# Performance work log

Hardware: AMD Instinct MI355X
Metric: run time of the kernel (lower is better)

The kernel has to match this reference:

```python
import jax, jax.numpy as jnp
import numpy as np


def _lstm_dir(x, Wih, Whh, bih, bhh, reverse):
    # x: [B,T,D]; Wih: [4H,D]; Whh: [4H,H]; PyTorch gate order i,f,g,o
    if reverse:
        x = x[:, ::-1, :]
    H = Whh.shape[1]
    B = x.shape[0]
    # precompute input projection for all timesteps: [B,T,4H]
    xW = jnp.einsum('btd,gd->btg', x, Wih) + bih + bhh
    xW = jnp.swapaxes(xW, 0, 1)  # [T,B,4H]
    h0 = jnp.zeros((B, H), x.dtype)
    c0 = jnp.zeros((B, H), x.dtype)

    def step(carry, xt):
        h, c = carry
        g = xt + h @ Whh.T
        i, f, gg, o = jnp.split(g, 4, axis=-1)
        c = jax.nn.sigmoid(f) * c + jax.nn.sigmoid(i) * jnp.tanh(gg)
        h = jax.nn.sigmoid(o) * jnp.tanh(c)
        return (h, c), h

    _, ys = jax.lax.scan(step, (h0, c0), xW)
    ys = jnp.swapaxes(ys, 0, 1)  # [B,T,H]
    if reverse:
        ys = ys[:, ::-1, :]
    return ys


def _bilstm(x, Wih_f, Whh_f, bih_f, bhh_f, Wih_b, Whh_b, bih_b, bhh_b):
    yf = _lstm_dir(x, Wih_f, Whh_f, bih_f, bhh_f, False)
    yb = _lstm_dir(x, Wih_b, Whh_b, bih_b, bhh_b, True)
    return jnp.concatenate([yf, yb], axis=-1)


def setup_inputs() -> dict:
    key = jax.random.key(0)
    B, T, D = 1024, 512, 30
    H1, H2, DENSE, OUT = 96, 64, 32, 1
    ks = jax.random.split(key, 21)

    def U(k, shape, fan):
        bnd = 1.0 / np.sqrt(fan)
        return jax.random.uniform(k, shape, jnp.float32, -bnd, bnd)

    x = jax.random.normal(ks[0], (B, T, D), jnp.float32)
    inp = {'x': x}
    # layer 1 (input D -> H1), forward and backward directions
    inp['Wih1f'] = U(ks[1], (4 * H1, D), H1)
    inp['Whh1f'] = U(ks[2], (4 * H1, H1), H1)
    inp['bih1f'] = U(ks[3], (4 * H1,), H1)
    inp['bhh1f'] = U(ks[4], (4 * H1,), H1)
    inp['Wih1b'] = U(ks[5], (4 * H1, D), H1)
    inp['Whh1b'] = U(ks[6], (4 * H1, H1), H1)
    inp['bih1b'] = U(ks[7], (4 * H1,), H1)
    inp['bhh1b'] = U(ks[8], (4 * H1,), H1)
    # layer 2 (input 2*H1 -> H2)
    inp['Wih2f'] = U(ks[9], (4 * H2, 2 * H1), H2)
    inp['Whh2f'] = U(ks[10], (4 * H2, H2), H2)
    inp['bih2f'] = U(ks[11], (4 * H2,), H2)
    inp['bhh2f'] = U(ks[12], (4 * H2,), H2)
    inp['Wih2b'] = U(ks[13], (4 * H2, 2 * H1), H2)
    inp['Whh2b'] = U(ks[14], (4 * H2, H2), H2)
    inp['bih2b'] = U(ks[15], (4 * H2,), H2)
    inp['bhh2b'] = U(ks[16], (4 * H2,), H2)
    # dense head
    inp['W1'] = U(ks[17], (DENSE, 2 * H2), 2 * H2)
    inp['b1'] = U(ks[18], (DENSE,), 2 * H2)
    inp['W2'] = U(ks[19], (OUT, DENSE), DENSE)
    inp['b2'] = U(ks[20], (OUT,), DENSE)
    return inp


def reference(x, Wih1f, Whh1f, bih1f, bhh1f, Wih1b, Whh1b, bih1b, bhh1b,
              Wih2f, Whh2f, bih2f, bhh2f, Wih2b, Whh2b, bih2b, bhh2b,
              W1, b1, W2, b2):
    # dropout layers are identity in eval mode
    h1 = _bilstm(x, Wih1f, Whh1f, bih1f, bhh1f, Wih1b, Whh1b, bih1b, bhh1b)   # [B,T,192]
    h2 = _bilstm(h1, Wih2f, Whh2f, bih2f, bhh2f, Wih2b, Whh2b, bih2b, bhh2b)  # [B,T,128]
    last = h2[:, -1, :]                       # [B,128]
    d = jax.nn.relu(last @ W1.T + b1)         # [B,32]
    return d @ W2.T + b2                      # [B,1]
```

## Files before the change

### kernel.cpp

```cpp
#include <hip/hip_runtime.h>
#include <math.h>

#define B_  1024
#define T_  512
#define D_  30
#define H1_ 96
#define G1_ 384
#define H2_ 64
#define G2_ 256

__device__ float g_h1[(size_t)B_ * T_ * 192];
__device__ float g_h2f[(size_t)B_ * H2_];

__device__ __forceinline__ float fast_tanh(float v) {
  float a = fabsf(v);
  float e = __expf(-2.0f * a);
  float t = 1.0f - 2.0f * e / (1.0f + e);
  return v < 0.0f ? -t : t;
}
__device__ __forceinline__ float fast_sigmoid(float v) {
  return 0.5f + 0.5f * fast_tanh(0.5f * v);
}

#define FMAROW(a_, w_, v_)                                                    \
  a_ = fmaf(w_.x, v_.x, a_); a_ = fmaf(w_.y, v_.y, a_);                       \
  a_ = fmaf(w_.z, v_.z, a_); a_ = fmaf(w_.w, v_.w, a_);

#define BAR_LGKM() do {                                                       \
    asm volatile("s_waitcnt lgkmcnt(0)" ::: "memory");                        \
    __builtin_amdgcn_s_barrier();                                             \
    asm volatile("" ::: "memory");                                            \
  } while (0)

__global__ __launch_bounds__(768, 4)
void lstm1_kernel(const float* __restrict__ x,
                  const float* __restrict__ Wih_f, const float* __restrict__ Whh_f,
                  const float* __restrict__ bih_f, const float* __restrict__ bhh_f,
                  const float* __restrict__ Wih_b, const float* __restrict__ Whh_b,
                  const float* __restrict__ bih_b, const float* __restrict__ bhh_b)
{
  const int tid = threadIdx.x;
  const int dir = blockIdx.y;
  const int b0  = blockIdx.x * 8;

  const float* __restrict__ Wih = dir ? Wih_b : Wih_f;
  const float* __restrict__ Whh = dir ? Whh_b : Whh_f;
  const float* __restrict__ bih = dir ? bih_b : bih_f;
  const float* __restrict__ bhh = dir ? bhh_b : bhh_f;

  const int j  = tid >> 3;
  const int e  = tid & 7;
  const int wv = tid >> 6;
  const int jl = j & 7;

  __shared__ __align__(16) float hxs[2 * 1056];
  __shared__ float4 scr4[12 * 584];

  float4 wA0,wA1,wA2,wA3, wB0,wB1,wB2,wB3, wC0,wC1,wC2,wC3, wD0,wD1,wD2,wD3;
  if (e < 2) {
    const int k0 = e * 16;
#define LDXF(r_, kk) (((kk) < D_) ? Wih[(r_) * D_ + (kk)] : 0.0f)
#define LW4(d0,d1,d2,d3, r_) {                                                \
    d0 = make_float4(LDXF(r_,k0+ 0),LDXF(r_,k0+ 1),LDXF(r_,k0+ 2),LDXF(r_,k0+ 3)); \
    d1 = make_float4(LDXF(r_,k0+ 4),LDXF(r_,k0+ 5),LDXF(r_,k0+ 6),LDXF(r_,k0+ 7)); \
    d2 = make_float4(LDXF(r_,k0+ 8),LDXF(r_,k0+ 9),LDXF(r_,k0+10),LDXF(r_,k0+11)); \
    d3 = make_float4(LDXF(r_,k0+12),LDXF(r_,k0+13),LDXF(r_,k0+14),LDXF(r_,k0+15)); }
    LW4(wA0,wA1,wA2,wA3, j      )
    LW4(wB0,wB1,wB2,wB3, j +  96)
    LW4(wC0,wC1,wC2,wC3, j + 192)
    LW4(wD0,wD1,wD2,wD3, j + 288)
#undef LW4
#undef LDXF
  } else {
    const int c0 = e * 16 - 32;
    const float4* pA = (const float4*)(Whh + (j      ) * H1_ + c0);
    const float4* pB = (const float4*)(Whh + (j +  96) * H1_ + c0);
    const float4* pC = (const float4*)(Whh + (j + 192) * H1_ + c0);
    const float4* pD = (const float4*)(Whh + (j + 288) * H1_ + c0);
    wA0=pA[0]; wA1=pA[1]; wA2=pA[2]; wA3=pA[3];
    wB0=pB[0]; wB1=pB[1]; wB2=pB[2]; wB3=pB[3];
    wC0=pC[0]; wC1=pC[1]; wC2=pC[2]; wC3=pC[3];
    wD0=pD[0]; wD1=pD[1]; wD2=pD[2]; wD3=pD[3];
  }

  const float bias_i = bih[j      ] + bhh[j      ];
  const float bias_f = bih[j +  96] + bhh[j +  96];
  const float bias_g = bih[j + 192] + bhh[j + 192];
  const float bias_o = bih[j + 288] + bhh[j + 288];
  float c_state = 0.0f;

  for (int i = tid; i < 2 * 1056; i += 768) hxs[i] = 0.0f;
  __syncthreads();
  const int xb = tid / 30;
  const int xd = tid - xb * 30;
  const int xoff = 132 * (xd >> 4) + 16 * xb + (xd & 15);
  if (tid < 240) {
    const int t0 = dir ? (T_ - 1) : 0;
    hxs[xoff] = x[((size_t)(b0 + xb) * T_ + t0) * D_ + xd];
  }
  __syncthreads();

  const int ef = 33 * e;
  float4* swp = scr4 + wv * 584 + jl * 73 + e;
  const float4* srd = scr4 + wv * 584 + jl * 73 + e * 9;
  const int hoff = 132 * (2 + (j >> 4)) + 16 * e + ((32 + j) & 15);
  float* __restrict__ gp = g_h1 + ((size_t)(b0 + e) * T_) * 192
                                + (size_t)dir * 96 + j;

  for (int s = 0; s < T_; ++s) {
    const int t   = dir ? (T_ - 1 - s) : s;
    const int cur = s & 1, nxt = cur ^ 1;
    float xn = 0.0f;
    if (tid < 240 && s + 1 < T_) {
      const int tn = dir ? (t - 1) : (t + 1);
      xn = x[((size_t)(b0 + xb) * T_ + tn) * D_ + xd];
    }
    const float4* hb = (const float4*)(hxs + cur * 1056);
    float aI0=0.f,aI1=0.f,aI2=0.f,aI3=0.f,aI4=0.f,aI5=0.f,aI6=0.f,aI7=0.f;
    float aF0=0.f,aF1=0.f,aF2=0.f,aF3=0.f,aF4=0.f,aF5=0.f,aF6=0.f,aF7=0.f;
    float aG0=0.f,aG1=0.f,aG2=0.f,aG3=0.f,aG4=0.f,aG5=0.f,aG6=0.f,aG7=0.f;
    float aO0=0.f,aO1=0.f,aO2=0.f,aO3=0.f,aO4=0.f,aO5=0.f,aO6=0.f,aO7=0.f;
#define FB1(i) {                                                              \
    float4 v0 = hb[ef +  0 + i]; float4 v1 = hb[ef +  4 + i];                 \
    float4 v2 = hb[ef +  8 + i]; float4 v3 = hb[ef + 12 + i];                 \
    float4 v4 = hb[ef + 16 + i]; float4 v5 = hb[ef + 20 + i];                 \
    float4 v6 = hb[ef + 24 + i]; float4 v7 = hb[ef + 28 + i];                 \
    FMAROW(aI0, wA##i, v0) FMAROW(aF0, wB##i, v0)                             \
    FMAROW(aG0, wC##i, v0) FMAROW(aO0, wD##i, v0)                             \
    FMAROW(aI1, wA##i, v1) FMAROW(aF1, wB##i, v1)                             \
    FMAROW(aG1, wC##i, v1) FMAROW(aO1, wD##i, v1)                             \
    FMAROW(aI2, wA##i, v2) FMAROW(aF2, wB##i, v2)                             \
    FMAROW(aG2, wC##i, v2) FMAROW(aO2, wD##i, v2)                             \
    FMAROW(aI3, wA##i, v3) FMAROW(aF3, wB##i, v3)                             \
    FMAROW(aG3, wC##i, v3) FMAROW(aO3, wD##i, v3)                             \
    FMAROW(aI4, wA##i, v4) FMAROW(aF4, wB##i, v4)                             \
    FMAROW(aG4, wC##i, v4) FMAROW(aO4, wD##i, v4)                             \
    FMAROW(aI5, wA##i, v5) FMAROW(aF5, wB##i, v5)                             \
    FMAROW(aG5, wC##i, v5) FMAROW(aO5, wD##i, v5)                             \
    FMAROW(aI6, wA##i, v6) FMAROW(aF6, wB##i, v6)                             \
    FMAROW(aG6, wC##i, v6) FMAROW(aO6, wD##i, v6)                             \
    FMAROW(aI7, wA##i, v7) FMAROW(aF7, wB##i, v7)                             \
    FMAROW(aG7, wC##i, v7) FMAROW(aO7, wD##i, v7) }
    FB1(0) FB1(1) FB1(2) FB1(3)
#undef FB1
    swp[0*9] = make_float4(aI0, aF0, aG0, aO0);
    swp[1*9] = make_float4(aI1, aF1, aG1, aO1);
    swp[2*9] = make_float4(aI2, aF2, aG2, aO2);
    swp[3*9] = make_float4(aI3, aF3, aG3, aO3);
    swp[4*9] = make_float4(aI4, aF4, aG4, aO4);
    swp[5*9] = make_float4(aI5, aF5, aG5, aO5);
    swp[6*9] = make_float4(aI6, aF6, aG6, aO6);
    swp[7*9] = make_float4(aI7, aF7, aG7, aO7);
    {
      float4 r0 = srd[0], r1 = srd[1], r2 = srd[2], r3 = srd[3];
      float4 r4 = srd[4], r5 = srd[5], r6 = srd[6], r7 = srd[7];
      float gi = bias_i + r0.x + r1.x + r2.x + r3.x + r4.x + r5.x + r6.x + r7.x;
      float gf = bias_f + r0.y + r1.y + r2.y + r3.y + r4.y + r5.y + r6.y + r7.y;
      float gg = bias_g + r0.z + r1.z + r2.z + r3.z + r4.z + r5.z + r6.z + r7.z;
      float go = bias_o + r0.w + r1.w + r2.w + r3.w + r4.w + r5.w + r6.w + r7.w;
      float iv = fast_sigmoid(gi);
      float fv = fast_sigmoid(gf);
      float ov = fast_sigmoid(go);
      c_state = fv * c_state + iv * fast_tanh(gg);
      float h = ov * fast_tanh(c_state);
      hxs[nxt * 1056 + hoff] = h;
      gp[(size_t)t * 192] = h;
    }
    if (tid < 240 && s + 1 < T_) hxs[nxt * 1056 + xoff] = xn;
    BAR_LGKM();
  }
}

__global__ __launch_bounds__(1024, 4)
void lstm2f_kernel(const float* __restrict__ Wih, const float* __restrict__ Whh,
                   const float* __restrict__ bih, const float* __restrict__ bhh)
{
  const int tid = threadIdx.x;
  const int b0  = blockIdx.x * 4;
  const int j   = tid >> 4;
  const int e   = tid & 15;
  const int wv  = tid >> 6;
  const int jl  = j & 3;

  __shared__ __align__(16) float hxs[2 * 1088];
  __shared__ float4 scr4[16 * 280];

  const int k0 = e * 16;
  float4 wA0,wA1,wA2,wA3, wB0,wB1,wB2,wB3, wC0,wC1,wC2,wC3, wD0,wD1,wD2,wD3;
  if (e < 12) {
    const float4* pA = (const float4*)(Wih + (j      ) * 192 + k0);
    const float4* pB = (const float4*)(Wih + (j +  64) * 192 + k0);
    const float4* pC = (const float4*)(Wih + (j + 128) * 192 + k0);
    const float4* pD = (const float4*)(Wih + (j + 192) * 192 + k0);
    wA0=pA[0]; wA1=pA[1]; wA2=pA[2]; wA3=pA[3];
    wB0=pB[0]; wB1=pB[1]; wB2=pB[2]; wB3=pB[3];
    wC0=pC[0]; wC1=pC[1]; wC2=pC[2]; wC3=pC[3];
    wD0=pD[0]; wD1=pD[1]; wD2=pD[2]; wD3=pD[3];
  } else {
    const int c0 = k0 - 192;
    const float4* pA = (const float4*)(Whh + (j      ) * H2_ + c0);
    const float4* pB = (const float4*)(Whh + (j +  64) * H2_ + c0);
    const float4* pC = (const float4*)(Whh + (j + 128) * H2_ + c0);
    const float4* pD = (const float4*)(Whh + (j + 192) * H2_ + c0);
    wA0=pA[0]; wA1=pA[1]; wA2=pA[2]; wA3=pA[3];
    wB0=pB[0]; wB1=pB[1]; wB2=pB[2]; wB3=pB[3];
    wC0=pC[0]; wC1=pC[1]; wC2=pC[2]; wC3=pC[3];
    wD0=pD[0]; wD1=pD[1]; wD2=pD[2]; wD3=pD[3];
  }

  const float bias_i = bih[j      ] + bhh[j      ];
  const float bias_f = bih[j +  64] + bhh[j +  64];
  const float bias_g = bih[j + 128] + bhh[j + 128];
  const float bias_o = bih[j + 192] + bhh[j + 192];
  float c_state = 0.0f;

  for (int i = tid; i < 2 * 1088; i += 1024) hxs[i] = 0.0f;
  __syncthreads();
  const int pb = tid / 96;
  const int pj = tid - pb * 96;
  const int soff = 68 * ((2 * pj) >> 4) + 16 * pb + ((2 * pj) & 15);
  if (tid < 384) {
    *(float2*)&hxs[soff] =
        *(const float2*)&g_h1[((size_t)(b0 + pb) * T_ + 0) * 192 + pj * 2];
  }
  __syncthreads();

  const int ef = 17 * e;
  float4* swp = scr4 + wv * 280 + jl * 70 + e;
  const float4* srd = scr4 + wv * 280 + jl * 70 + e * 17;
  const int hoff = 68 * (12 + (j >> 4)) + 16 * e + (j & 15);

  for (int s = 0; s < T_; ++s) {
    const int cur = s & 1, nxt = cur ^ 1;
    float2 pre = make_float2(0.0f, 0.0f);
    if (tid < 384 && s + 1 < T_) {
      pre = *(const float2*)&g_h1[((size_t)(b0 + pb) * T_ + (s + 1)) * 192 + pj * 2];
    }
    const float4* hb = (const float4*)(hxs + cur * 1088);
    float aI0=0.f,aI1=0.f,aI2=0.f,aI3=0.f;
    float aF0=0.f,aF1=0.f,aF2=0.f,aF3=0.f;
    float aG0=0.f,aG1=0.f,aG2=0.f,aG3=0.f;
    float aO0=0.f,aO1=0.f,aO2=0.f,aO3=0.f;
#define FB2(i) {                                                              \
    float4 v0 = hb[ef + 0 + i]; float4 v1 = hb[ef + 4 + i];                   \
    float4 v2 = hb[ef + 8 + i]; float4 v3 = hb[ef + 12 + i];                  \
    FMAROW(aI0, wA##i, v0) FMAROW(aF0, wB##i, v0)                             \
    FMAROW(aG0, wC##i, v0) FMAROW(aO0, wD##i, v0)                             \
    FMAROW(aI1, wA##i, v1) FMAROW(aF1, wB##i, v1)                             \
    FMAROW(aG1, wC##i, v1) FMAROW(aO1, wD##i, v1)                             \
    FMAROW(aI2, wA##i, v2) FMAROW(aF2, wB##i, v2)                             \
    FMAROW(aG2, wC##i, v2) FMAROW(aO2, wD##i, v2)                             \
    FMAROW(aI3, wA##i, v3) FMAROW(aF3, wB##i, v3)                             \
    FMAROW(aG3, wC##i, v3) FMAROW(aO3, wD##i, v3) }
    FB2(0) FB2(1) FB2(2) FB2(3)
#undef FB2
    swp[0*17] = make_float4(aI0, aF0, aG0, aO0);
    swp[1*17] = make_float4(aI1, aF1, aG1, aO1);
    swp[2*17] = make_float4(aI2, aF2, aG2, aO2);
    swp[3*17] = make_float4(aI3, aF3, aG3, aO3);
    if (e < 4) {
      float gi = bias_i, gf = bias_f, gg = bias_g, go = bias_o;
#pragma unroll
      for (int k = 0; k < 16; ++k) {
        float4 r = srd[k];
        gi += r.x; gf += r.y; gg += r.z; go += r.w;
      }
      float iv = fast_sigmoid(gi), fv = fast_sigmoid(gf), ov = fast_sigmoid(go);
      c_state = fv * c_state + iv * fast_tanh(gg);
      float h = ov * fast_tanh(c_state);
      hxs[nxt * 1088 + hoff] = h;
      if (s == T_ - 1) g_h2f[(b0 + e) * H2_ + j] = h;
    }
    if (tid < 384 && s + 1 < T_) *(float2*)&hxs[nxt * 1088 + soff] = pre;
    BAR_LGKM();
  }
}

__global__ __launch_bounds__(256)
void tail_kernel(const float* __restrict__ Wih, const float* __restrict__ bih,
                 const float* __restrict__ bhh,
                 const float* __restrict__ W1, const float* __restrict__ b1,
                 const float* __restrict__ W2, const float* __restrict__ b2,
                 float* __restrict__ out)
{
  const int tid = threadIdx.x;
  const int b0  = blockIdx.x * 8;

  __shared__ __align__(16) float hl[8][192];
  __shared__ float gb[G2_ * 9];
  __shared__ __align__(16) float last[8][128];
  __shared__ float db[8][32];

  for (int i = tid; i < 8 * 96; i += 256) {
    int bb = i / 96, jj = i - (i / 96) * 96;
    *(float2*)&hl[bb][jj * 2] =
        *(const float2*)&g_h1[((size_t)(b0 + bb) * T_ + (T_ - 1)) * 192 + jj * 2];
  }
  for (int i = tid; i < 8 * 64; i += 256) {
    int bb = i >> 6, jj = i & 63;
    last[bb][jj] = g_h2f[(b0 + bb) * H2_ + jj];
  }
  __syncthreads();

  {
    const int gg_ = tid;
    const float* wr = Wih + gg_ * 192;
    const float bias = bih[gg_] + bhh[gg_];
    float acc[8];
#pragma unroll
    for (int b = 0; b < 8; ++b) acc[b] = bias;
#pragma unroll 4
    for (int qq = 0; qq < 48; ++qq) {
      float4 wv = *(const float4*)&wr[qq * 4];
#pragma unroll
      for (int b = 0; b < 8; ++b) {
        float4 v = *(const float4*)&hl[b][qq * 4];
        acc[b] = fmaf(wv.x, v.x, acc[b]);
        acc[b] = fmaf(wv.y, v.y, acc[b]);
        acc[b] = fmaf(wv.z, v.z, acc[b]);
        acc[b] = fmaf(wv.w, v.w, acc[b]);
      }
    }
#pragma unroll
    for (int b = 0; b < 8; ++b) gb[gg_ * 9 + b] = acc[b];
  }
  __syncthreads();

  for (int p = tid; p < 512; p += 256) {
    int jj = p & 63, bb = p >> 6;
    float gi = gb[(jj      ) * 9 + bb];
    float gg = gb[(jj + 128) * 9 + bb];
    float go = gb[(jj + 192) * 9 + bb];
    float c  = fast_sigmoid(gi) * fast_tanh(gg);
    float h  = fast_sigmoid(go) * fast_tanh(c);
    last[bb][64 + jj] = h;
  }
  __syncthreads();

  {
    int u = tid & 31, bb = tid >> 5;
    const float* wr1 = W1 + u * 128;
    float a = b1[u];
#pragma unroll
    for (int qq = 0; qq < 32; ++qq) {
      float4 wv = *(const float4*)&wr1[qq * 4];
      float4 v  = *(const float4*)&last[bb][qq * 4];
      a = fmaf(wv.x, v.x, a); a = fmaf(wv.y, v.y, a);
      a = fmaf(wv.z, v.z, a); a = fmaf(wv.w, v.w, a);
    }
    db[bb][u] = fmaxf(a, 0.0f);
  }
  __syncthreads();

  if (tid < 8) {
    float a = b2[0];
#pragma unroll
    for (int u2 = 0; u2 < 32; ++u2) a = fmaf(db[tid][u2], W2[u2], a);
    out[b0 + tid] = a;
  }
}

extern "C" void kernel_launch(void* const* d_in, const int* in_sizes, int n_in,
                              void* d_out, int out_size, void* d_ws, size_t ws_size,
                              hipStream_t stream)
{
  const float* x     = (const float*)d_in[0];
  const float* Wih1f = (const float*)d_in[1];
  const float* Whh1f = (const float*)d_in[2];
  const float* bih1f = (const float*)d_in[3];
  const float* bhh1f = (const float*)d_in[4];
  const float* Wih1b = (const float*)d_in[5];
  const float* Whh1b = (const float*)d_in[6];
  const float* bih1b = (const float*)d_in[7];
  const float* bhh1b = (const float*)d_in[8];
  const float* Wih2f = (const float*)d_in[9];
  const float* Whh2f = (const float*)d_in[10];
  const float* bih2f = (const float*)d_in[11];
  const float* bhh2f = (const float*)d_in[12];
  const float* Wih2b = (const float*)d_in[13];
  const float* bih2b = (const float*)d_in[15];
  const float* bhh2b = (const float*)d_in[16];
  const float* W1    = (const float*)d_in[17];
  const float* b1    = (const float*)d_in[18];
  const float* W2    = (const float*)d_in[19];
  const float* b2    = (const float*)d_in[20];

  (void)d_ws; (void)ws_size; (void)in_sizes; (void)n_in; (void)out_size;

  lstm1_kernel<<<dim3(128, 2), 768, 0, stream>>>(
      x, Wih1f, Whh1f, bih1f, bhh1f, Wih1b, Whh1b, bih1b, bhh1b);
  lstm2f_kernel<<<256, 1024, 0, stream>>>(
      Wih2f, Whh2f, bih2f, bhh2f);
  tail_kernel<<<128, 256, 0, stream>>>(
      Wih2b, bih2b, bhh2b, W1, b1, W2, b2, (float*)d_out);
}
```

Baseline: 2.996 ms.

## Restructure layer-2 LSTM thread mapping and split gate scratch into per-gate planes

The layer-1 kernel now writes partial gate sums as scalars into four separate per-gate planes instead of interleaved float4s, so the reduction reads are spread differently across LDS banks. The layer-2 kernel is remapped so each thread handles two gate rows over a 32-wide K slice for 4 batches. It uses a single hidden/input buffer and a padded 33-stride gate scratch, with 256 threads doing the cell update. This drops the double buffer and adds a second barrier per timestep, trading more sync for a different LDS access pattern and reduction fan-in.

New measurement: 2.756 ms. -8.0%, faster.

```diff
diff --git a/kernel.cpp b/kernel.cpp
--- a/kernel.cpp
+++ b/kernel.cpp
@@ -54,7 +54,7 @@
   const int jl = j & 7;
 
   __shared__ __align__(16) float hxs[2 * 1056];
-  __shared__ float4 scr4[12 * 584];
+  __shared__ float scr[12 * 2336];
 
   float4 wA0,wA1,wA2,wA3, wB0,wB1,wB2,wB3, wC0,wC1,wC2,wC3, wD0,wD1,wD2,wD3;
   if (e < 2) {
@@ -101,8 +101,8 @@
   __syncthreads();
 
   const int ef = 33 * e;
-  float4* swp = scr4 + wv * 584 + jl * 73 + e;
-  const float4* srd = scr4 + wv * 584 + jl * 73 + e * 9;
+  float* swp = scr + wv * 2336 + jl * 72 + e;
+  const float* srd = scr + wv * 2336 + jl * 72 + e * 9;
   const int hoff = 132 * (2 + (j >> 4)) + 16 * e + ((32 + j) & 15);
   float* __restrict__ gp = g_h1 + ((size_t)(b0 + e) * T_) * 192
                                 + (size_t)dir * 96 + j;
@@ -143,21 +143,35 @@
     FMAROW(aG7, wC##i, v7) FMAROW(aO7, wD##i, v7) }
     FB1(0) FB1(1) FB1(2) FB1(3)
 #undef FB1
-    swp[0*9] = make_float4(aI0, aF0, aG0, aO0);
-    swp[1*9] = make_float4(aI1, aF1, aG1, aO1);
-    swp[2*9] = make_float4(aI2, aF2, aG2, aO2);
-    swp[3*9] = make_float4(aI3, aF3, aG3, aO3);
-    swp[4*9] = make_float4(aI4, aF4, aG4, aO4);
-    swp[5*9] = make_float4(aI5, aF5, aG5, aO5);
-    swp[6*9] = make_float4(aI6, aF6, aG6, aO6);
-    swp[7*9] = make_float4(aI7, aF7, aG7, aO7);
+    swp[0*584 + 0*9] = aI0; swp[0*584 + 1*9] = aI1;
+    swp[0*584 + 2*9] = aI2; swp[0*584 + 3*9] = aI3;
+    swp[0*584 + 4*9] = aI4; swp[0*584 + 5*9] = aI5;
+    swp[0*584 + 6*9] = aI6; swp[0*584 + 7*9] = aI7;
+    swp[1*584 + 0*9] = aF0; swp[1*584 + 1*9] = aF1;
+    swp[1*584 + 2*9] = aF2; swp[1*584 + 3*9] = aF3;
+    swp[1*584 + 4*9] = aF4; swp[1*584 + 5*9] = aF5;
+    swp[1*584 + 6*9] = aF6; swp[1*584 + 7*9] = aF7;
+    swp[2*584 + 0*9] = aG0; swp[2*584 + 1*9] = aG1;
+    swp[2*584 + 2*9] = aG2; swp[2*584 + 3*9] = aG3;
+    swp[2*584 + 4*9] = aG4; swp[2*584 + 5*9] = aG5;
+    swp[2*584 + 6*9] = aG6; swp[2*584 + 7*9] = aG7;
+    swp[3*584 + 0*9] = aO0; swp[3*584 + 1*9] = aO1;
+    swp[3*584 + 2*9] = aO2; swp[3*584 + 3*9] = aO3;
+    swp[3*584 + 4*9] = aO4; swp[3*584 + 5*9] = aO5;
+    swp[3*584 + 6*9] = aO6; swp[3*584 + 7*9] = aO7;
     {
-      float4 r0 = srd[0], r1 = srd[1], r2 = srd[2], r3 = srd[3];
-      float4 r4 = srd[4], r5 = srd[5], r6 = srd[6], r7 = srd[7];
-      float gi = bias_i + r0.x + r1.x + r2.x + r3.x + r4.x + r5.x + r6.x + r7.x;
-      float gf = bias_f + r0.y + r1.y + r2.y + r3.y + r4.y + r5.y + r6.y + r7.y;
-      float gg = bias_g + r0.z + r1.z + r2.z + r3.z + r4.z + r5.z + r6.z + r7.z;
-      float go = bias_o + r0.w + r1.w + r2.w + r3.w + r4.w + r5.w + r6.w + r7.w;
+      float gi = bias_i + srd[0*584+0] + srd[0*584+1] + srd[0*584+2]
+               + srd[0*584+3] + srd[0*584+4] + srd[0*584+5]
+               + srd[0*584+6] + srd[0*584+7];
+      float gf = bias_f + srd[1*584+0] + srd[1*584+1] + srd[1*584+2]
+               + srd[1*584+3] + srd[1*584+4] + srd[1*584+5]
+               + srd[1*584+6] + srd[1*584+7];
+      float gg = bias_g + srd[2*584+0] + srd[2*584+1] + srd[2*584+2]
+               + srd[2*584+3] + srd[2*584+4] + srd[2*584+5]
+               + srd[2*584+6] + srd[2*584+7];
+      float go = bias_o + srd[3*584+0] + srd[3*584+1] + srd[3*584+2]
+               + srd[3*584+3] + srd[3*584+4] + srd[3*584+5]
+               + srd[3*584+6] + srd[3*584+7];
       float iv = fast_sigmoid(gi);
       float fv = fast_sigmoid(gf);
       float ov = fast_sigmoid(go);
@@ -177,101 +191,88 @@
 {
   const int tid = threadIdx.x;
   const int b0  = blockIdx.x * 4;
-  const int j   = tid >> 4;
-  const int e   = tid & 15;
-  const int wv  = tid >> 6;
-  const int jl  = j & 3;
-
-  __shared__ __align__(16) float hxs[2 * 1088];
-  __shared__ float4 scr4[16 * 280];
-
-  const int k0 = e * 16;
-  float4 wA0,wA1,wA2,wA3, wB0,wB1,wB2,wB3, wC0,wC1,wC2,wC3, wD0,wD1,wD2,wD3;
-  if (e < 12) {
-    const float4* pA = (const float4*)(Wih + (j      ) * 192 + k0);
-    const float4* pB = (const float4*)(Wih + (j +  64) * 192 + k0);
-    const float4* pC = (const float4*)(Wih + (j + 128) * 192 + k0);
-    const float4* pD = (const float4*)(Wih + (j + 192) * 192 + k0);
-    wA0=pA[0]; wA1=pA[1]; wA2=pA[2]; wA3=pA[3];
-    wB0=pB[0]; wB1=pB[1]; wB2=pB[2]; wB3=pB[3];
-    wC0=pC[0]; wC1=pC[1]; wC2=pC[2]; wC3=pC[3];
-    wD0=pD[0]; wD1=pD[1]; wD2=pD[2]; wD3=pD[3];
-  } else {
-    const int c0 = k0 - 192;
-    const float4* pA = (const float4*)(Whh + (j      ) * H2_ + c0);
-    const float4* pB = (const float4*)(Whh + (j +  64) * H2_ + c0);
-    const float4* pC = (const float4*)(Whh + (j + 128) * H2_ + c0);
-    const float4* pD = (const float4*)(Whh + (j + 192) * H2_ + c0);
-    wA0=pA[0]; wA1=pA[1]; wA2=pA[2]; wA3=pA[3];
-    wB0=pB[0]; wB1=pB[1]; wB2=pB[2]; wB3=pB[3];
-    wC0=pC[0]; wC1=pC[1]; wC2=pC[2]; wC3=pC[3];
-    wD0=pD[0]; wD1=pD[1]; wD2=pD[2]; wD3=pD[3];
-  }
-
-  const float bias_i = bih[j      ] + bhh[j      ];
-  const float bias_f = bih[j +  64] + bhh[j +  64];
-  const float bias_g = bih[j + 128] + bhh[j + 128];
-  const float bias_o = bih[j + 192] + bhh[j + 192];
+  const int jj  = tid % 128;
+  const int e   = tid / 128;
+
+  __shared__ __align__(16) float hx[4][256];
+  __shared__ float gbuf[G2_ * 33];
+
+  float4 w0,w1,w2,w3,w4,w5,w6,w7,w8,w9,w10,w11,w12,w13,w14,w15;
+  {
+    const float4* wa = (e < 6) ? (const float4*)(Wih + jj * 192 + 32 * e)
+                               : (const float4*)(Whh + jj * H2_ + 32 * (e - 6));
+    w0 = wa[0];  w1 = wa[1];  w2 = wa[2];  w3 = wa[3];
+    w4 = wa[4];  w5 = wa[5];  w6 = wa[6];  w7 = wa[7];
+    const float4* wb = (e < 6) ? (const float4*)(Wih + (jj + 128) * 192 + 32 * e)
+                               : (const float4*)(Whh + (jj + 128) * H2_ + 32 * (e - 6));
+    w8  = wb[0]; w9  = wb[1]; w10 = wb[2]; w11 = wb[3];
+    w12 = wb[4]; w13 = wb[5]; w14 = wb[6]; w15 = wb[7];
+  }
+
+  const int uj = tid & 63;
+  const int ub = (tid >> 6) & 3;
+  const float bias_i = bih[uj      ] + bhh[uj      ];
+  const float bias_f = bih[uj +  64] + bhh[uj +  64];
+  const float bias_g = bih[uj + 128] + bhh[uj + 128];
+  const float bias_o = bih[uj + 192] + bhh[uj + 192];
   float c_state = 0.0f;
 
-  for (int i = tid; i < 2 * 1088; i += 1024) hxs[i] = 0.0f;
+  for (int i = tid; i < 4 * 256; i += 1024) (&hx[0][0])[i] = 0.0f;
   __syncthreads();
   const int pb = tid / 96;
   const int pj = tid - pb * 96;
-  const int soff = 68 * ((2 * pj) >> 4) + 16 * pb + ((2 * pj) & 15);
   if (tid < 384) {
-    *(float2*)&hxs[soff] =
+    *(float2*)&hx[pb][pj * 2] =
         *(const float2*)&g_h1[((size_t)(b0 + pb) * T_ + 0) * 192 + pj * 2];
   }
   __syncthreads();
 
-  const int ef = 17 * e;
-  float4* swp = scr4 + wv * 280 + jl * 70 + e;
-  const float4* srd = scr4 + wv * 280 + jl * 70 + e * 17;
-  const int hoff = 68 * (12 + (j >> 4)) + 16 * e + (j & 15);
+  const int eoff = e * 8;
+  const float4* hx4 = (const float4*)(&hx[0][0]);
 
   for (int s = 0; s < T_; ++s) {
-    const int cur = s & 1, nxt = cur ^ 1;
     float2 pre = make_float2(0.0f, 0.0f);
     if (tid < 384 && s + 1 < T_) {
       pre = *(const float2*)&g_h1[((size_t)(b0 + pb) * T_ + (s + 1)) * 192 + pj * 2];
     }
-    const float4* hb = (const float4*)(hxs + cur * 1088);
-    float aI0=0.f,aI1=0.f,aI2=0.f,aI3=0.f;
-    float aF0=0.f,aF1=0.f,aF2=0.f,aF3=0.f;
-    float aG0=0.f,aG1=0.f,aG2=0.f,aG3=0.f;
-    float aO0=0.f,aO1=0.f,aO2=0.f,aO3=0.f;
-#define FB2(i) {                                                              \
-    float4 v0 = hb[ef + 0 + i]; float4 v1 = hb[ef + 4 + i];                   \
-    float4 v2 = hb[ef + 8 + i]; float4 v3 = hb[ef + 12 + i];                  \
-    FMAROW(aI0, wA##i, v0) FMAROW(aF0, wB##i, v0)                             \
-    FMAROW(aG0, wC##i, v0) FMAROW(aO0, wD##i, v0)                             \
-    FMAROW(aI1, wA##i, v1) FMAROW(aF1, wB##i, v1)                             \
-    FMAROW(aG1, wC##i, v1) FMAROW(aO1, wD##i, v1)                             \
-    FMAROW(aI2, wA##i, v2) FMAROW(aF2, wB##i, v2)                             \
-    FMAROW(aG2, wC##i, v2) FMAROW(aO2, wD##i, v2)                             \
-    FMAROW(aI3, wA##i, v3) FMAROW(aF3, wB##i, v3)                             \
-    FMAROW(aG3, wC##i, v3) FMAROW(aO3, wD##i, v3) }
-    FB2(0) FB2(1) FB2(2) FB2(3)
+    float accA0=0.f, accA1=0.f, accA2=0.f, accA3=0.f;
+    float accB0=0.f, accB1=0.f, accB2=0.f, accB3=0.f;
+#define FB2(i, k) {                                                           \
+    float4 v0 = hx4[0*64 + eoff + i]; float4 v1 = hx4[1*64 + eoff + i];       \
+    float4 v2 = hx4[2*64 + eoff + i]; float4 v3 = hx4[3*64 + eoff + i];       \
+    FMAROW(accA0, w##i, v0) FMAROW(accB0, w##k, v0)                           \
+    FMAROW(accA1, w##i, v1) FMAROW(accB1, w##k, v1)                           \
+    FMAROW(accA2, w##i, v2) FMAROW(accB2, w##k, v2)                           \
+    FMAROW(accA3, w##i, v3) FMAROW(accB3, w##k, v3) }
+    FB2(0,8) FB2(1,9) FB2(2,10) FB2(3,11)
+    FB2(4,12) FB2(5,13) FB2(6,14) FB2(7,15)
 #undef FB2
-    swp[0*17] = make_float4(aI0, aF0, aG0, aO0);
-    swp[1*17] = make_float4(aI1, aF1, aG1, aO1);
-    swp[2*17] = make_float4(aI2, aF2, aG2, aO2);
-    swp[3*17] = make_float4(aI3, aF3, aG3, aO3);
-    if (e < 4) {
+    {
+      const int ga = jj * 33 + e;
+      gbuf[ga +  0] = accA0; gbuf[ga +  8] = accA1;
+      gbuf[ga + 16] = accA2; gbuf[ga + 24] = accA3;
+      const int gbB = (jj + 128) * 33 + e;
+      gbuf[gbB +  0] = accB0; gbuf[gbB +  8] = accB1;
+      gbuf[gbB + 16] = accB2; gbuf[gbB + 24] = accB3;
+    }
+    BAR_LGKM();
+    if (tid < 384 && s + 1 < T_) *(float2*)&hx[pb][pj * 2] = pre;
+    if (tid < 256) {
+      const int ro = ub * 8;
       float gi = bias_i, gf = bias_f, gg = bias_g, go = bias_o;
 #pragma unroll
-      for (int k = 0; k < 16; ++k) {
-        float4 r = srd[k];
-        gi += r.x; gf += r.y; gg += r.z; go += r.w;
+      for (int ee = 0; ee < 8; ++ee) {
+        gi += gbuf[(uj      ) * 33 + ro + ee];
+        gf += gbuf[(uj +  64) * 33 + ro + ee];
+        gg += gbuf[(uj + 128) * 33 + ro + ee];
+        go += gbuf[(uj + 192) * 33 + ro + ee];
       }
       float iv = fast_sigmoid(gi), fv = fast_sigmoid(gf), ov = fast_sigmoid(go);
       c_state = fv * c_state + iv * fast_tanh(gg);
       float h = ov * fast_tanh(c_state);
-      hxs[nxt * 1088 + hoff] = h;
-      if (s == T_ - 1) g_h2f[(b0 + e) * H2_ + j] = h;
-    }
-    if (tid < 384 && s + 1 < T_) *(float2*)&hxs[nxt * 1088 + soff] = pre;
+      hx[ub][192 + uj] = h;
+      if (s == T_ - 1) g_h2f[(b0 + ub) * H2_ + uj] = h;
+    }
     BAR_LGKM();
   }
 }
```
